# Optimization experiments

Hardware: AMD Instinct MI355X
Metric: run time of the kernel (lower is better)

The kernel has to match this reference:

```python
import jax, jax.numpy as jnp
import numpy as np

N_SUPPORT = 8192
N_QUERY = 8192
INPUT_DIM = 1024
EMBED_DIM = 512
N_CLASSES = 64


def setup_inputs() -> dict:
    key = jax.random.key(0)
    k1, k2, k3, k4 = jax.random.split(key, 4)
    support_data = jax.random.normal(k1, (N_SUPPORT, INPUT_DIM), dtype=jnp.float32)
    query_data = jax.random.normal(k2, (N_QUERY, INPUT_DIM), dtype=jnp.float32)
    support_labels = jax.random.randint(k3, (N_SUPPORT,), 0, N_CLASSES, dtype=jnp.int32)
    W = jax.random.normal(k4, (INPUT_DIM, EMBED_DIM), dtype=jnp.float32) * (1.0 / np.sqrt(INPUT_DIM))
    return {"support_data": support_data, "support_labels": support_labels,
            "query_data": query_data, "W": W}


def _l2_normalize(x, eps=1e-12):
    # Matches F.normalize(p=2): x / max(||x||, eps)
    n = jnp.linalg.norm(x, axis=-1, keepdims=True)
    return x / jnp.maximum(n, eps)


def reference(support_data, support_labels, query_data, W):
    # encoder: single linear projection
    s_emb = support_data @ W            # [Ns, D]
    q_emb = query_data @ W              # [Nq, D]
    s_norm = _l2_normalize(s_emb)
    q_norm = _l2_normalize(q_emb)
    # cosine similarities for all query/support pairs: [Nq, Ns]
    sims = q_norm @ s_norm.T
    # per-class sum over support samples (torch.unique -> sorted 0..N_CLASSES-1)
    # segment_sum along the support axis: [N_classes, Nq] -> [Nq, N_classes]
    class_scores = jax.ops.segment_sum(sims.T, support_labels, num_segments=N_CLASSES).T
    return jax.nn.softmax(class_scores, axis=-1)
```

## Files before the change

kernel.cpp:

```cpp
#include <hip/hip_runtime.h>
#include <hip/hip_bf16.h>

#define NS 8192
#define NQ 8192
#define NTOT 16384
#define KDIM 1024
#define ED 512
#define NC 64

typedef __attribute__((ext_vector_type(4))) float fx4;
typedef __attribute__((ext_vector_type(8))) short sx8;
typedef __attribute__((ext_vector_type(8))) unsigned short ux8;

__device__ __forceinline__ unsigned short f2bf(float f) {
  union { float f; unsigned u; } v; v.f = f;
  unsigned r = v.u + 0x7fffu + ((v.u >> 16) & 1u);
  return (unsigned short)(r >> 16);
}
__device__ __forceinline__ float bf2f(unsigned short h) {
  union { unsigned u; float f; } v; v.u = ((unsigned)h) << 16;
  return v.f;
}

__global__ __launch_bounds__(256) void k_prep(
    const float* __restrict__ W, unsigned short* __restrict__ Wtp,
    float* __restrict__ rowssq, float* __restrict__ Pacc) {
  int c = blockIdx.x * 256 + threadIdx.x;
  int lane = c & 63;
  int j    = (c >> 6) & 3;
  int s2   = (c >> 8) & 1;
  int kt   = (c >> 9) & 15;
  int n64  = c >> 13;
  int quad = lane >> 4, ml = lane & 15;
  int n  = n64 * 64 + j * 16 + ml;
  int kb = kt * 64 + (s2 * 4 + quad) * 8;
  ux8 o;
#pragma unroll
  for (int e = 0; e < 8; ++e) o[e] = f2bf(W[(size_t)(kb + e) * ED + n]);
  *(ux8*)&Wtp[(size_t)c * 8] = o;
  if (c < NTOT) rowssq[c] = 0.f;
  if (c < NC * ED) Pacc[c] = 0.f;
}

__global__ __launch_bounds__(256, 4) void k_gemm_embed(
    const float* __restrict__ Xs, const float* __restrict__ Xq,
    const unsigned short* __restrict__ Wtp,
    unsigned short* __restrict__ emb, float* __restrict__ rowssq) {
  __shared__ unsigned short Ash[2][64 * 8 * 8];

  int lid = blockIdx.x;
  int x = lid & 7;
  int s = lid >> 3;
  int m_blk = x * 32 + (s >> 2);
  int n_blk = s & 3;

  const float* Xsrc = (m_blk < 128)
      ? (Xs + (size_t)m_blk * 64 * KDIM)
      : (Xq + (size_t)(m_blk - 128) * 64 * KDIM);

  int t = threadIdx.x;
  int lane = t & 63, w = t >> 6;
  int quad = lane >> 4, ml = lane & 15;
  int n64 = n_blk * 2 + (w >> 1);
  int jb = (w & 1) * 2;

  const unsigned short* Bbase = Wtp + ((size_t)n64 * 8192 + lane) * 8;

  fx4 acc[4][2];
#pragma unroll
  for (int i = 0; i < 4; ++i)
#pragma unroll
    for (int j = 0; j < 2; ++j) acc[i][j] = fx4{0.f, 0.f, 0.f, 0.f};

  fx4 avA[2][2], avB[2][2];
  sx8 bfA[2][2], bfB[2][2];

  auto loadA = [&](int kt, fx4 (&av)[2][2]) {
    int k0 = kt * 64;
#pragma unroll
    for (int c = 0; c < 2; ++c) {
      int ch = t + 256 * c;
      int m = ch >> 3, kq = ch & 7;
      const float* g = &Xsrc[(size_t)m * KDIM + k0 + kq * 8];
      av[c][0] = *(const fx4*)g;
      av[c][1] = *(const fx4*)(g + 4);
    }
  };
  auto writeA = [&](const fx4 (&av)[2][2], int bbuf) {
#pragma unroll
    for (int c = 0; c < 2; ++c) {
      int ch = t + 256 * c;
      int m = ch >> 3, kq = ch & 7;
      ux8 o;
      o[0] = f2bf(av[c][0].x); o[1] = f2bf(av[c][0].y);
      o[2] = f2bf(av[c][0].z); o[3] = f2bf(av[c][0].w);
      o[4] = f2bf(av[c][1].x); o[5] = f2bf(av[c][1].y);
      o[6] = f2bf(av[c][1].z); o[7] = f2bf(av[c][1].w);
      *(ux8*)&Ash[bbuf][((m * 8) + (kq ^ (m & 7))) * 8] = o;
    }
  };
  auto loadB = [&](int kt, sx8 (&bf)[2][2]) {
#pragma unroll
    for (int s2 = 0; s2 < 2; ++s2)
#pragma unroll
      for (int j = 0; j < 2; ++j)
        bf[s2][j] = *(const sx8*)&Bbase[(size_t)(kt * 512 + s2 * 256 + (jb + j) * 64) * 8];
  };
  auto compute = [&](int b, const sx8 (&bf)[2][2]) {
#pragma unroll
    for (int s2 = 0; s2 < 2; ++s2) {
      int kq = s2 * 4 + quad;
      sx8 af[4];
#pragma unroll
      for (int i = 0; i < 4; ++i) {
        int row = i * 16 + ml;
        af[i] = *(const sx8*)&Ash[b][(row * 8 + (kq ^ (row & 7))) * 8];
      }
#pragma unroll
      for (int i = 0; i < 4; ++i)
#pragma unroll
        for (int j = 0; j < 2; ++j)
          acc[i][j] = __builtin_amdgcn_mfma_f32_16x16x32_bf16(af[i], bf[s2][j], acc[i][j], 0, 0, 0);
    }
  };
  auto sync_step = [&]() {
    __builtin_amdgcn_sched_barrier(0);
    asm volatile("s_waitcnt lgkmcnt(0)" ::: "memory");
    __builtin_amdgcn_s_barrier();
    __builtin_amdgcn_sched_barrier(0);
  };

  loadB(0, bfA);
  loadA(0, avA);
  loadA(1, avB);
  writeA(avA, 0);
  sync_step();

  for (int it = 0; it < 8; ++it) {
    int kt0 = it * 2;
    loadB(kt0 + 1, bfB);
    loadA(kt0 + 2 < 16 ? kt0 + 2 : 15, avA);
    compute(0, bfA);
    writeA(avB, 1);
    sync_step();

    loadB(kt0 + 2 < 16 ? kt0 + 2 : 15, bfA);
    loadA(kt0 + 3 < 16 ? kt0 + 3 : 15, avB);
    compute(1, bfB);
    writeA(avA, 0);
    sync_step();
  }

  int grow = m_blk * 64;
  int gcol = n_blk * 128 + w * 32;
#pragma unroll
  for (int i = 0; i < 4; ++i) {
#pragma unroll
    for (int r = 0; r < 4; ++r) {
      int mrow = grow + i * 16 + quad * 4 + r;
      float p = 0.f;
#pragma unroll
      for (int j = 0; j < 2; ++j) {
        emb[(size_t)mrow * ED + gcol + j * 16 + ml] = f2bf(acc[i][j][r]);
        p += acc[i][j][r] * acc[i][j][r];
      }
#pragma unroll
      for (int off = 1; off < 16; off <<= 1) p += __shfl_xor(p, off, 16);
      if (ml == 0) atomicAdd(&rowssq[mrow], p);
    }
  }
}

__global__ __launch_bounds__(256) void k_proto(
    const unsigned short* __restrict__ embS, const float* __restrict__ rowssq,
    const int* __restrict__ labels, float* __restrict__ Pacc) {
  __shared__ float Pl[NC * 64];
  int t = threadIdx.x;
#pragma unroll
  for (int i = 0; i < 16; ++i) Pl[i * 256 + t] = 0.f;
  __syncthreads();

  int w = t >> 6, lane = t & 63;
  int ds = blockIdx.y;
  int row0 = blockIdx.x * 256;
#pragma unroll 4
  for (int r = w; r < 256; r += 4) {
    int row = row0 + r;
    int lbl = labels[row];
    float scale = 1.0f / fmaxf(sqrtf(rowssq[row]), 1e-12f);
    float v = bf2f(embS[(size_t)row * ED + ds * 64 + lane]) * scale;
    atomicAdd(&Pl[lbl * 64 + lane], v);
  }
  __syncthreads();

#pragma unroll
  for (int i = 0; i < 16; ++i) {
    int idx = i * 256 + t;
    atomicAdd(&Pacc[(size_t)(idx >> 6) * ED + ds * 64 + (idx & 63)], Pl[idx]);
  }
}

__global__ __launch_bounds__(256) void k_scores(
    const unsigned short* __restrict__ embQ, const float* __restrict__ ssqQ,
    const float* __restrict__ Pacc, float* __restrict__ out) {
  __shared__ unsigned short Pl[4096 * 8];
  int t = threadIdx.x;
#pragma unroll
  for (int i = 0; i < 16; ++i) {
    int c = t + 256 * i;
    int cls = c & 63, ks = c >> 6;
    const float* p = &Pacc[(size_t)cls * ED + ks * 8];
    fx4 p0 = *(const fx4*)p;
    fx4 p1 = *(const fx4*)(p + 4);
    ux8 bb;
    bb[0] = f2bf(p0.x); bb[1] = f2bf(p0.y); bb[2] = f2bf(p0.z); bb[3] = f2bf(p0.w);
    bb[4] = f2bf(p1.x); bb[5] = f2bf(p1.y); bb[6] = f2bf(p1.z); bb[7] = f2bf(p1.w);
    *(ux8*)&Pl[(size_t)c * 8] = bb;
  }
  __syncthreads();

  int w = t >> 6, lane = t & 63;
  int quad = lane >> 4, ml = lane & 15;
  int qrow0 = blockIdx.x * 64 + w * 16;

  fx4 acc[4];
#pragma unroll
  for (int i = 0; i < 4; ++i) acc[i] = fx4{0.f, 0.f, 0.f, 0.f};

#pragma unroll 4
  for (int ki = 0; ki < 16; ++ki) {
    sx8 a = *(const sx8*)&embQ[(size_t)(qrow0 + ml) * ED + ki * 32 + quad * 8];
#pragma unroll
    for (int nt = 0; nt < 4; ++nt) {
      sx8 b = *(const sx8*)&Pl[((ki * 4 + quad) * 64 + nt * 16 + ml) * 8];
      acc[nt] = __builtin_amdgcn_mfma_f32_16x16x32_bf16(a, b, acc[nt], 0, 0, 0);
    }
  }

#pragma unroll
  for (int r = 0; r < 4; ++r) {
    int qq = qrow0 + quad * 4 + r;
    float scale = 1.0f / fmaxf(sqrtf(ssqQ[qq]), 1e-12f);
    float s[4];
#pragma unroll
    for (int nt = 0; nt < 4; ++nt) s[nt] = acc[nt][r] * scale;
    float m = fmaxf(fmaxf(s[0], s[1]), fmaxf(s[2], s[3]));
#pragma unroll
    for (int off = 1; off < 16; off <<= 1) m = fmaxf(m, __shfl_xor(m, off, 16));
    float e[4], ssum = 0.f;
#pragma unroll
    for (int nt = 0; nt < 4; ++nt) { e[nt] = __expf(s[nt] - m); ssum += e[nt]; }
#pragma unroll
    for (int off = 1; off < 16; off <<= 1) ssum += __shfl_xor(ssum, off, 16);
    float inv = 1.0f / ssum;
#pragma unroll
    for (int nt = 0; nt < 4; ++nt)
      out[(size_t)qq * NC + nt * 16 + ml] = e[nt] * inv;
  }
}

extern "C" void kernel_launch(void* const* d_in, const int* in_sizes, int n_in,
                              void* d_out, int out_size, void* d_ws, size_t ws_size,
                              hipStream_t stream) {
  const float* Xs     = (const float*)d_in[0];
  const int*   labels = (const int*)d_in[1];
  const float* Xq     = (const float*)d_in[2];
  const float* W      = (const float*)d_in[3];
  float* out = (float*)d_out;

  char* ws = (char*)d_ws;
  size_t off = 0;
  unsigned short* Wtp = (unsigned short*)(ws + off); off += (size_t)ED * KDIM * 2;
  unsigned short* emb = (unsigned short*)(ws + off); off += (size_t)NTOT * ED * 2;
  float* rowssq = (float*)(ws + off); off += (size_t)NTOT * 4;
  float* Pacc   = (float*)(ws + off); off += (size_t)NC * ED * 4;

  k_prep<<<256, 256, 0, stream>>>(W, Wtp, rowssq, Pacc);
  k_gemm_embed<<<1024, 256, 0, stream>>>(Xs, Xq, Wtp, emb, rowssq);
  k_proto<<<dim3(32, 8), 256, 0, stream>>>(emb, rowssq, labels, Pacc);
  k_scores<<<NQ / 64, 256, 0, stream>>>(emb + (size_t)NS * ED, rowssq + NS, Pacc, out);
}
```

Baseline: 174.1 us.

## Double GEMM K-tile to 128 and halve occupancy target in embed kernel

The embedding GEMM now stages 128-wide K tiles of the fp32 inputs, converted to bf16 in shared memory, instead of 64-wide ones. This halves the number of main-loop iterations and block barriers. B fragments are no longer prefetched one step ahead; they are loaded at the start of each step, just before compute. Launch bounds drop from 4 to 2 blocks per CU so the larger register set for A prefetch and B fragments fits. The risk is lower occupancy and exposed B load latency.

```diff
diff --git a/kernel.cpp b/kernel.cpp
--- a/kernel.cpp
+++ b/kernel.cpp
@@ -42,11 +42,11 @@
   if (c < NC * ED) Pacc[c] = 0.f;
 }
 
-__global__ __launch_bounds__(256, 4) void k_gemm_embed(
+__global__ __launch_bounds__(256, 2) void k_gemm_embed(
     const float* __restrict__ Xs, const float* __restrict__ Xq,
     const unsigned short* __restrict__ Wtp,
     unsigned short* __restrict__ emb, float* __restrict__ rowssq) {
-  __shared__ unsigned short Ash[2][64 * 8 * 8];
+  __shared__ unsigned short Ash[2][2][64 * 8 * 8];
 
   int lid = blockIdx.x;
   int x = lid & 7;
@@ -72,55 +72,59 @@
 #pragma unroll
     for (int j = 0; j < 2; ++j) acc[i][j] = fx4{0.f, 0.f, 0.f, 0.f};
 
-  fx4 avA[2][2], avB[2][2];
-  sx8 bfA[2][2], bfB[2][2];
-
-  auto loadA = [&](int kt, fx4 (&av)[2][2]) {
-    int k0 = kt * 64;
-#pragma unroll
-    for (int c = 0; c < 2; ++c) {
-      int ch = t + 256 * c;
-      int m = ch >> 3, kq = ch & 7;
-      const float* g = &Xsrc[(size_t)m * KDIM + k0 + kq * 8];
+  fx4 avA[4][2], avB[4][2];
+
+  int tkq = t & 15;
+  int thalf = tkq >> 3, toct = tkq & 7;
+
+  auto loadA = [&](int kt, fx4 (&av)[4][2]) {
+    int k0 = kt * 128;
+#pragma unroll
+    for (int c = 0; c < 4; ++c) {
+      int m = (t >> 4) + 16 * c;
+      const float* g = &Xsrc[(size_t)m * KDIM + k0 + tkq * 8];
       av[c][0] = *(const fx4*)g;
       av[c][1] = *(const fx4*)(g + 4);
     }
   };
-  auto writeA = [&](const fx4 (&av)[2][2], int bbuf) {
-#pragma unroll
-    for (int c = 0; c < 2; ++c) {
-      int ch = t + 256 * c;
-      int m = ch >> 3, kq = ch & 7;
+  auto writeA = [&](const fx4 (&av)[4][2], int bbuf) {
+#pragma unroll
+    for (int c = 0; c < 4; ++c) {
+      int m = (t >> 4) + 16 * c;
       ux8 o;
       o[0] = f2bf(av[c][0].x); o[1] = f2bf(av[c][0].y);
       o[2] = f2bf(av[c][0].z); o[3] = f2bf(av[c][0].w);
       o[4] = f2bf(av[c][1].x); o[5] = f2bf(av[c][1].y);
       o[6] = f2bf(av[c][1].z); o[7] = f2bf(av[c][1].w);
-      *(ux8*)&Ash[bbuf][((m * 8) + (kq ^ (m & 7))) * 8] = o;
-    }
-  };
-  auto loadB = [&](int kt, sx8 (&bf)[2][2]) {
-#pragma unroll
-    for (int s2 = 0; s2 < 2; ++s2)
-#pragma unroll
-      for (int j = 0; j < 2; ++j)
-        bf[s2][j] = *(const sx8*)&Bbase[(size_t)(kt * 512 + s2 * 256 + (jb + j) * 64) * 8];
-  };
-  auto compute = [&](int b, const sx8 (&bf)[2][2]) {
-#pragma unroll
-    for (int s2 = 0; s2 < 2; ++s2) {
-      int kq = s2 * 4 + quad;
+      *(ux8*)&Ash[bbuf][thalf][((m * 8) + (toct ^ (m & 7))) * 8] = o;
+    }
+  };
+  auto loadB = [&](int kt, sx8 (&bf)[4][2]) {
+#pragma unroll
+    for (int s2g = 0; s2g < 4; ++s2g)
+#pragma unroll
+      for (int j = 0; j < 2; ++j) {
+        int kt64 = 2 * kt + (s2g >> 1);
+        int s2p = s2g & 1;
+        bf[s2g][j] = *(const sx8*)&Bbase[(size_t)(kt64 * 512 + s2p * 256 + (jb + j) * 64) * 8];
+      }
+  };
+  auto compute = [&](int b, const sx8 (&bf)[4][2]) {
+#pragma unroll
+    for (int s2g = 0; s2g < 4; ++s2g) {
+      int kq16 = s2g * 4 + quad;
+      int half = kq16 >> 3, oct = kq16 & 7;
       sx8 af[4];
 #pragma unroll
       for (int i = 0; i < 4; ++i) {
         int row = i * 16 + ml;
-        af[i] = *(const sx8*)&Ash[b][(row * 8 + (kq ^ (row & 7))) * 8];
+        af[i] = *(const sx8*)&Ash[b][half][(row * 8 + (oct ^ (row & 7))) * 8];
       }
 #pragma unroll
       for (int i = 0; i < 4; ++i)
 #pragma unroll
         for (int j = 0; j < 2; ++j)
-          acc[i][j] = __builtin_amdgcn_mfma_f32_16x16x32_bf16(af[i], bf[s2][j], acc[i][j], 0, 0, 0);
+          acc[i][j] = __builtin_amdgcn_mfma_f32_16x16x32_bf16(af[i], bf[s2g][j], acc[i][j], 0, 0, 0);
     }
   };
   auto sync_step = [&]() {
@@ -130,25 +134,29 @@
     __builtin_amdgcn_sched_barrier(0);
   };
 
-  loadB(0, bfA);
   loadA(0, avA);
   loadA(1, avB);
   writeA(avA, 0);
   sync_step();
 
-  for (int it = 0; it < 8; ++it) {
+  for (int it = 0; it < 4; ++it) {
     int kt0 = it * 2;
-    loadB(kt0 + 1, bfB);
-    loadA(kt0 + 2 < 16 ? kt0 + 2 : 15, avA);
-    compute(0, bfA);
-    writeA(avB, 1);
-    sync_step();
-
-    loadB(kt0 + 2 < 16 ? kt0 + 2 : 15, bfA);
-    loadA(kt0 + 3 < 16 ? kt0 + 3 : 15, avB);
-    compute(1, bfB);
-    writeA(avA, 0);
-    sync_step();
+    {
+      sx8 bf[4][2];
+      loadB(kt0, bf);
+      loadA(kt0 + 2 < 8 ? kt0 + 2 : 7, avA);
+      compute(0, bf);
+      writeA(avB, 1);
+      sync_step();
+    }
+    {
+      sx8 bf[4][2];
+      loadB(kt0 + 1, bf);
+      loadA(kt0 + 3 < 8 ? kt0 + 3 : 7, avB);
+      compute(1, bf);
+      writeA(avA, 0);
+      sync_step();
+    }
   }
 
   int grow = m_blk * 64;
```

After: 170.2 us. -2.2%, faster.

## Compute full embedding width per block to convert and load X once

Applied to the files above, without the earlier changes.

The embedding GEMM now uses 256 blocks of 512 threads, each owning 64 rows and all 512 output columns, instead of 1024 blocks that each covered a quarter of the columns. Each row tile of fp32 input is read and converted to bf16 only once rather than four times, which cuts global traffic and conversion work on the A side. In exchange each wave holds twice the accumulators, B-fragment prefetch across stages is dropped (B is loaded just before use), and with 256 blocks on 256 CUs occupancy and latency hiding are lower.

```diff
diff --git a/kernel.cpp b/kernel.cpp
--- a/kernel.cpp
+++ b/kernel.cpp
@@ -42,18 +42,13 @@
   if (c < NC * ED) Pacc[c] = 0.f;
 }
 
-__global__ __launch_bounds__(256, 4) void k_gemm_embed(
+__global__ __launch_bounds__(512, 2) void k_gemm_embed(
     const float* __restrict__ Xs, const float* __restrict__ Xq,
     const unsigned short* __restrict__ Wtp,
     unsigned short* __restrict__ emb, float* __restrict__ rowssq) {
   __shared__ unsigned short Ash[2][64 * 8 * 8];
 
-  int lid = blockIdx.x;
-  int x = lid & 7;
-  int s = lid >> 3;
-  int m_blk = x * 32 + (s >> 2);
-  int n_blk = s & 3;
-
+  int m_blk = blockIdx.x;
   const float* Xsrc = (m_blk < 128)
       ? (Xs + (size_t)m_blk * 64 * KDIM)
       : (Xq + (size_t)(m_blk - 128) * 64 * KDIM);
@@ -61,52 +56,40 @@
   int t = threadIdx.x;
   int lane = t & 63, w = t >> 6;
   int quad = lane >> 4, ml = lane & 15;
-  int n64 = n_blk * 2 + (w >> 1);
-  int jb = (w & 1) * 2;
-
-  const unsigned short* Bbase = Wtp + ((size_t)n64 * 8192 + lane) * 8;
-
-  fx4 acc[4][2];
+
+  const unsigned short* Bbase = Wtp + ((size_t)w * 8192 + lane) * 8;
+
+  fx4 acc[4][4];
 #pragma unroll
   for (int i = 0; i < 4; ++i)
 #pragma unroll
-    for (int j = 0; j < 2; ++j) acc[i][j] = fx4{0.f, 0.f, 0.f, 0.f};
-
-  fx4 avA[2][2], avB[2][2];
-  sx8 bfA[2][2], bfB[2][2];
-
-  auto loadA = [&](int kt, fx4 (&av)[2][2]) {
-    int k0 = kt * 64;
-#pragma unroll
-    for (int c = 0; c < 2; ++c) {
-      int ch = t + 256 * c;
-      int m = ch >> 3, kq = ch & 7;
-      const float* g = &Xsrc[(size_t)m * KDIM + k0 + kq * 8];
-      av[c][0] = *(const fx4*)g;
-      av[c][1] = *(const fx4*)(g + 4);
-    }
-  };
-  auto writeA = [&](const fx4 (&av)[2][2], int bbuf) {
-#pragma unroll
-    for (int c = 0; c < 2; ++c) {
-      int ch = t + 256 * c;
-      int m = ch >> 3, kq = ch & 7;
-      ux8 o;
-      o[0] = f2bf(av[c][0].x); o[1] = f2bf(av[c][0].y);
-      o[2] = f2bf(av[c][0].z); o[3] = f2bf(av[c][0].w);
-      o[4] = f2bf(av[c][1].x); o[5] = f2bf(av[c][1].y);
-      o[6] = f2bf(av[c][1].z); o[7] = f2bf(av[c][1].w);
-      *(ux8*)&Ash[bbuf][((m * 8) + (kq ^ (m & 7))) * 8] = o;
-    }
-  };
-  auto loadB = [&](int kt, sx8 (&bf)[2][2]) {
+    for (int j = 0; j < 4; ++j) acc[i][j] = fx4{0.f, 0.f, 0.f, 0.f};
+
+  fx4 avA[2], avB[2];
+
+  int am = t >> 3, akq = t & 7;
+
+  auto loadA = [&](int kt, fx4 (&av)[2]) {
+    const float* g = &Xsrc[(size_t)am * KDIM + kt * 64 + akq * 8];
+    av[0] = *(const fx4*)g;
+    av[1] = *(const fx4*)(g + 4);
+  };
+  auto writeA = [&](const fx4 (&av)[2], int bbuf) {
+    ux8 o;
+    o[0] = f2bf(av[0].x); o[1] = f2bf(av[0].y);
+    o[2] = f2bf(av[0].z); o[3] = f2bf(av[0].w);
+    o[4] = f2bf(av[1].x); o[5] = f2bf(av[1].y);
+    o[6] = f2bf(av[1].z); o[7] = f2bf(av[1].w);
+    *(ux8*)&Ash[bbuf][((am * 8) + (akq ^ (am & 7))) * 8] = o;
+  };
+  auto loadB = [&](int kt, sx8 (&bf)[2][4]) {
 #pragma unroll
     for (int s2 = 0; s2 < 2; ++s2)
 #pragma unroll
-      for (int j = 0; j < 2; ++j)
-        bf[s2][j] = *(const sx8*)&Bbase[(size_t)(kt * 512 + s2 * 256 + (jb + j) * 64) * 8];
-  };
-  auto compute = [&](int b, const sx8 (&bf)[2][2]) {
+      for (int j = 0; j < 4; ++j)
+        bf[s2][j] = *(const sx8*)&Bbase[(size_t)(kt * 512 + s2 * 256 + j * 64) * 8];
+  };
+  auto compute = [&](int b, const sx8 (&bf)[2][4]) {
 #pragma unroll
     for (int s2 = 0; s2 < 2; ++s2) {
       int kq = s2 * 4 + quad;
@@ -119,7 +102,7 @@
 #pragma unroll
       for (int i = 0; i < 4; ++i)
 #pragma unroll
-        for (int j = 0; j < 2; ++j)
+        for (int j = 0; j < 4; ++j)
           acc[i][j] = __builtin_amdgcn_mfma_f32_16x16x32_bf16(af[i], bf[s2][j], acc[i][j], 0, 0, 0);
     }
   };
@@ -130,7 +113,6 @@
     __builtin_amdgcn_sched_barrier(0);
   };
 
-  loadB(0, bfA);
   loadA(0, avA);
   loadA(1, avB);
   writeA(avA, 0);
@@ -138,21 +120,26 @@
 
   for (int it = 0; it < 8; ++it) {
     int kt0 = it * 2;
-    loadB(kt0 + 1, bfB);
-    loadA(kt0 + 2 < 16 ? kt0 + 2 : 15, avA);
-    compute(0, bfA);
-    writeA(avB, 1);
-    sync_step();
-
-    loadB(kt0 + 2 < 16 ? kt0 + 2 : 15, bfA);
-    loadA(kt0 + 3 < 16 ? kt0 + 3 : 15, avB);
-    compute(1, bfB);
-    writeA(avA, 0);
-    sync_step();
+    {
+      sx8 bf[2][4];
+      loadB(kt0, bf);
+      loadA(kt0 + 2 < 16 ? kt0 + 2 : 15, avA);
+      compute(0, bf);
+      writeA(avB, 1);
+      sync_step();
+    }
+    {
+      sx8 bf[2][4];
+      loadB(kt0 + 1, bf);
+      loadA(kt0 + 3 < 16 ? kt0 + 3 : 15, avB);
+      compute(1, bf);
+      writeA(avA, 0);
+      sync_step();
+    }
   }
 
   int grow = m_blk * 64;
-  int gcol = n_blk * 128 + w * 32;
+  int gcol = w * 64;
 #pragma unroll
   for (int i = 0; i < 4; ++i) {
 #pragma unroll
@@ -160,7 +147,7 @@
       int mrow = grow + i * 16 + quad * 4 + r;
       float p = 0.f;
 #pragma unroll
-      for (int j = 0; j < 2; ++j) {
+      for (int j = 0; j < 4; ++j) {
         emb[(size_t)mrow * ED + gcol + j * 16 + ml] = f2bf(acc[i][j][r]);
         p += acc[i][j][r] * acc[i][j][r];
       }
@@ -276,7 +263,7 @@
   float* Pacc   = (float*)(ws + off); off += (size_t)NC * ED * 4;
 
   k_prep<<<256, 256, 0, stream>>>(W, Wtp, rowssq, Pacc);
-  k_gemm_embed<<<1024, 256, 0, stream>>>(Xs, Xq, Wtp, emb, rowssq);
+  k_gemm_embed<<<256, 512, 0, stream>>>(Xs, Xq, Wtp, emb, rowssq);
   k_proto<<<dim3(32, 8), 256, 0, stream>>>(emb, rowssq, labels, Pacc);
   k_scores<<<NQ / 64, 256, 0, stream>>>(emb + (size_t)NS * ED, rowssq + NS, Pacc, out);
 }
```

Result: faster. 159.9 us (-8.1%).
